# Kernel tuning notes

Measured on AMD Instinct MI355X. Metric: run time of the kernel, lower is better.

Reference implementation:

```python
import jax, jax.numpy as jnp
import numpy as np

TEMP = 0.05          # self.temp
NUM_LABELED = 15080  # SysuDataset bank size


def setup_inputs() -> dict:
    key = jax.random.key(0)
    k1, k2, k3, k4, k5 = jax.random.split(key, 5)
    B, D, L = 512, 2048, NUM_LABELED
    f = jax.random.normal(k1, (B, D), jnp.float32)
    features = f / jnp.linalg.norm(f, axis=1, keepdims=True)  # L2-normalized embeddings
    fk = jax.random.normal(k2, (B, D), jnp.float32)
    features_k = fk / jnp.linalg.norm(fk, axis=1, keepdims=True)
    gt_labels = jax.random.randint(k3, (B, 5), 0, L)   # last column = pid index
    gt_labels_k = jax.random.randint(k4, (B, 5), 0, L)
    bank = jax.random.normal(k5, (L, D), jnp.float32)
    bank_features = bank / jnp.linalg.norm(bank, axis=1, keepdims=True)
    return {"features": features, "features_k": features_k,
            "gt_labels": gt_labels, "gt_labels_k": gt_labels_k,
            "bank_features": bank_features}


def reference(features, features_k, gt_labels, gt_labels_k, bank_features):
    # pids = cat([i[:, -1] for i in gt_labels]); all >= 0 by construction, so the
    # pids > -1 filter is an identity (static shapes under jit).
    pids = gt_labels[:, -1]                                  # [B]
    # HM.forward: inputs.mm(features.t()), then /= temp
    sim_all = (features @ bank_features.T) / TEMP            # [B, L]
    # segment-mean of logits grouped by memory label (labels == arange -> identity,
    # kept for faithfulness to the index_add / nums normalization in the source)
    labels = jnp.arange(NUM_LABELED)
    sim = jax.ops.segment_sum(sim_all.T, labels, num_segments=NUM_LABELED)  # [L, B]
    nums = jax.ops.segment_sum(jnp.ones((NUM_LABELED, 1), jnp.float32),
                               labels, num_segments=NUM_LABELED)            # [L, 1]
    sim = sim / nums
    logits = sim.T                                           # [B, L]
    logp = jax.nn.log_softmax(logits, axis=-1)
    loss = -jnp.mean(jnp.take_along_axis(logp, pids[:, None], axis=1))
    return loss
```

## Files before the change

### kernel.cpp

```cpp
#include <hip/hip_runtime.h>
#include <hip/hip_bf16.h>

#define M_ROWS 512
#define N_COLS 15080
#define K_DIM  2048
#define BM 128
#define BN 128
#define BKF 64
#define NT 118
#define KSTEPS (K_DIM / BKF)
#define SCALE 20.0f

typedef _Float16 f16x8 __attribute__((ext_vector_type(8)));
typedef float    f32x4 __attribute__((ext_vector_type(4)));

extern "C" __global__ __launch_bounds__(512, 4)
void k_gemm_lse(const float* __restrict__ A,
                const float* __restrict__ Bk,
                const int*   __restrict__ gt,
                float* __restrict__ pm,
                float* __restrict__ ps,
                float* __restrict__ tv)
{
    __shared__ __align__(16) ushort lds[16384];

    const int t  = threadIdx.x;
    const int bx = blockIdx.x;

    int mi, nt;
    if (bx < 448) {
        const int slot = bx & 7;
        const int rest = bx >> 3;
        mi = rest & 3;
        nt = (rest >> 2) * 8 + slot;
    } else {
        const int r2 = bx - 448;
        mi = r2 & 3;
        nt = 112 + (r2 >> 2);
    }
    const int rowA0 = mi * BM;
    const int rowB0 = nt * BN;

    int arow[2], ag[2];
#pragma unroll
    for (int i = 0; i < 2; i++) { int G = t + i * 512; arow[i] = G >> 3; ag[i] = G & 7; }

    float4 ra[4], rb[4];
    auto LOAD = [&](int kt) {
#pragma unroll
        for (int i = 0; i < 2; i++) {
            const float* pa = A + (size_t)(rowA0 + arow[i]) * K_DIM + kt * BKF + ag[i] * 8;
            ra[2 * i]     = *(const float4*)(pa);
            ra[2 * i + 1] = *(const float4*)(pa + 4);
            const int br = rowB0 + arow[i];
            if (br < N_COLS) {
                const float* pb = Bk + (size_t)br * K_DIM + kt * BKF + ag[i] * 8;
                rb[2 * i]     = *(const float4*)(pb);
                rb[2 * i + 1] = *(const float4*)(pb + 4);
            } else {
                rb[2 * i]     = make_float4(0.f, 0.f, 0.f, 0.f);
                rb[2 * i + 1] = make_float4(0.f, 0.f, 0.f, 0.f);
            }
        }
    };
    auto STORE = [&]() {
#pragma unroll
        for (int i = 0; i < 2; i++) {
            const int ba = (arow[i] * 128 + ag[i] * 16) ^ ((arow[i] & 7) << 4);
            f16x8 ha, hb;
            float4 x = ra[2 * i], y = ra[2 * i + 1];
            ha[0] = (_Float16)x.x; ha[1] = (_Float16)x.y; ha[2] = (_Float16)x.z; ha[3] = (_Float16)x.w;
            ha[4] = (_Float16)y.x; ha[5] = (_Float16)y.y; ha[6] = (_Float16)y.z; ha[7] = (_Float16)y.w;
            x = rb[2 * i]; y = rb[2 * i + 1];
            hb[0] = (_Float16)x.x; hb[1] = (_Float16)x.y; hb[2] = (_Float16)x.z; hb[3] = (_Float16)x.w;
            hb[4] = (_Float16)y.x; hb[5] = (_Float16)y.y; hb[6] = (_Float16)y.z; hb[7] = (_Float16)y.w;
            *(f16x8*)((char*)lds + ba)         = ha;
            *(f16x8*)((char*)lds + 16384 + ba) = hb;
        }
    };

    const int lane = t & 63;
    const int wid  = t >> 6;
    const int wm = wid >> 2, wn = wid & 3;
    const int q = lane >> 4, r = lane & 15;
    int aaddr[4][2], baddr[2][2];
#pragma unroll
    for (int m = 0; m < 4; m++) {
        const int rowa = wm * 64 + m * 16 + r;
#pragma unroll
        for (int ks = 0; ks < 2; ks++)
            aaddr[m][ks] = (rowa * 128 + ks * 64 + q * 16) ^ ((rowa & 7) << 4);
    }
#pragma unroll
    for (int n = 0; n < 2; n++) {
        const int rowb = wn * 32 + n * 16 + r;
#pragma unroll
        for (int ks = 0; ks < 2; ks++)
            baddr[n][ks] = 16384 + ((rowb * 128 + ks * 64 + q * 16) ^ ((rowb & 7) << 4));
    }

    f32x4 acc[4][2];
    const f32x4 zero = {0.f, 0.f, 0.f, 0.f};
#pragma unroll
    for (int m = 0; m < 4; m++)
#pragma unroll
        for (int n = 0; n < 2; n++) acc[m][n] = zero;

    LOAD(0);
    for (int kt = 0; kt < KSTEPS; kt++) {
        __syncthreads();
        STORE();
        __syncthreads();
        if (kt + 1 < KSTEPS) LOAD(kt + 1);

        f16x8 bf[2][2];
#pragma unroll
        for (int n = 0; n < 2; n++)
#pragma unroll
            for (int ks = 0; ks < 2; ks++)
                bf[n][ks] = *(const f16x8*)((const char*)lds + baddr[n][ks]);
#pragma unroll
        for (int m = 0; m < 4; m++) {
            const f16x8 af0 = *(const f16x8*)((const char*)lds + aaddr[m][0]);
            const f16x8 af1 = *(const f16x8*)((const char*)lds + aaddr[m][1]);
#pragma unroll
            for (int n = 0; n < 2; n++) {
                acc[m][n] = __builtin_amdgcn_mfma_f32_16x16x32_f16(af0, bf[n][0], acc[m][n], 0, 0, 0);
                acc[m][n] = __builtin_amdgcn_mfma_f32_16x16x32_f16(af1, bf[n][1], acc[m][n], 0, 0, 0);
            }
        }
    }

    __syncthreads();
    float* redm = (float*)lds;
    float* reds = ((float*)lds) + 512;

#pragma unroll
    for (int m = 0; m < 4; m++) {
#pragma unroll
        for (int j = 0; j < 4; j++) {
            const int lrow = wm * 64 + m * 16 + q * 4 + j;
            const int grow = rowA0 + lrow;
            const int pid  = gt[grow * 5 + 4];
            float sv[2];
            float mx = -INFINITY;
#pragma unroll
            for (int n = 0; n < 2; n++) {
                const int gc = rowB0 + wn * 32 + n * 16 + r;
                float s = SCALE * acc[m][n][j];
                s = (gc < N_COLS) ? s : -INFINITY;
                sv[n] = s;
                mx = fmaxf(mx, s);
                if (gc == pid) tv[grow] = s;
            }
#pragma unroll
            for (int d = 1; d < 16; d <<= 1) mx = fmaxf(mx, __shfl_xor(mx, d, 16));
            float se = 0.f;
#pragma unroll
            for (int n = 0; n < 2; n++) se += __expf(sv[n] - mx);
#pragma unroll
            for (int d = 1; d < 16; d <<= 1) se += __shfl_xor(se, d, 16);
            if (r == 0) { redm[wn * 128 + lrow] = mx; reds[wn * 128 + lrow] = se; }
        }
    }
    __syncthreads();
    if (t < 128) {
        float Mv = -INFINITY;
#pragma unroll
        for (int c = 0; c < 4; c++) Mv = fmaxf(Mv, redm[c * 128 + t]);
        float Sv = 0.f;
#pragma unroll
        for (int c = 0; c < 4; c++) Sv += reds[c * 128 + t] * __expf(redm[c * 128 + t] - Mv);
        pm[(rowA0 + t) * NT + nt] = Mv;
        ps[(rowA0 + t) * NT + nt] = Sv;
    }
}

extern "C" __global__ __launch_bounds__(128)
void k_rowlse(const float* __restrict__ pm,
              const float* __restrict__ ps,
              const float* __restrict__ tv,
              float* __restrict__ rowloss)
{
    const int b = blockIdx.x;
    const int i = threadIdx.x;
    __shared__ float wred[4];

    const float m = (i < NT) ? pm[b * NT + i] : -INFINITY;
    const float s = (i < NT) ? ps[b * NT + i] : 0.f;

    float M = m;
#pragma unroll
    for (int d = 1; d < 64; d <<= 1) M = fmaxf(M, __shfl_xor(M, d, 64));
    if ((i & 63) == 0) wred[i >> 6] = M;
    __syncthreads();
    M = fmaxf(wred[0], wred[1]);
    __syncthreads();

    float e = (i < NT) ? s * __expf(m - M) : 0.f;
#pragma unroll
    for (int d = 1; d < 64; d <<= 1) e += __shfl_xor(e, d, 64);
    if ((i & 63) == 0) wred[i >> 6] = e;
    __syncthreads();
    if (i == 0) {
        const float S = wred[0] + wred[1];
        rowloss[b] = M + logf(S) - tv[b];
    }
}

extern "C" __global__ __launch_bounds__(512)
void k_final(const float* __restrict__ rowloss, float* __restrict__ out)
{
    __shared__ float red[512];
    const int b = threadIdx.x;
    red[b] = rowloss[b];
    __syncthreads();
    for (int s = 256; s > 0; s >>= 1) {
        if (b < s) red[b] += red[b + s];
        __syncthreads();
    }
    if (b == 0) out[0] = red[0] / 512.0f;
}

extern "C" void kernel_launch(void* const* d_in, const int* in_sizes, int n_in,
                              void* d_out, int out_size, void* d_ws, size_t ws_size,
                              hipStream_t stream)
{
    const float* feat = (const float*)d_in[0];
    const int*   gt   = (const int*)d_in[2];
    const float* bank = (const float*)d_in[4];

    float* pm = (float*)d_ws;
    float* ps = pm + 512 * NT;
    float* tv = ps + 512 * NT;
    float* rl = tv + 512;

    k_gemm_lse<<<dim3(4 * NT), 512, 0, stream>>>(feat, bank, gt, pm, ps, tv);
    k_rowlse<<<dim3(512), 128, 0, stream>>>(pm, ps, tv, rl);
    k_final<<<dim3(1), 512, 0, stream>>>(rl, (float*)d_out);
}
```

Measured before the change: 250.1 us.

## Split GEMM along K into two slices and move LSE into separate reduction pass

Adds a split-K GEMM kernel that computes two K halves as separate workgroups (944 blocks of 256 threads, 4x4 MFMA tiles per wave) and writes raw partial logits to a padded workspace. A new row kernel sums the two partials, applies the scale and does an online log-sum-exp plus target lookup. The aim is more workgroups and better CU fill than the 472-block fused kernel. The cost is writing and rereading about 62 MB of partials through global memory, and the path only runs if the workspace is large enough.

```diff
diff --git a/kernel.cpp b/kernel.cpp
--- a/kernel.cpp
+++ b/kernel.cpp
@@ -3,16 +3,196 @@
 
 #define M_ROWS 512
 #define N_COLS 15080
+#define N_PAD  15104
 #define K_DIM  2048
 #define BM 128
 #define BN 128
 #define BKF 64
 #define NT 118
-#define KSTEPS (K_DIM / BKF)
 #define SCALE 20.0f
+
+#define KS 2
+#define KSLICE (K_DIM / KS)
+#define KSTEPS_SK (KSLICE / BKF)
 
 typedef _Float16 f16x8 __attribute__((ext_vector_type(8)));
 typedef float    f32x4 __attribute__((ext_vector_type(4)));
+
+extern "C" __global__ __launch_bounds__(256, 2)
+void k_gemm_sk(const float* __restrict__ A,
+               const float* __restrict__ Bk,
+               float* __restrict__ part)
+{
+    __shared__ __align__(16) ushort lds[16384];
+
+    const int t  = threadIdx.x;
+    const int bx = blockIdx.x;
+
+    const int wgid  = (bx & 7) * 118 + (bx >> 3);
+    const int mi    = wgid & 3;
+    const int group = wgid >> 2;
+    const int nt    = group >> 1;
+    const int ks    = group & 1;
+    const int rowA0 = mi * BM;
+    const int rowB0 = nt * BN;
+    const int kbase = ks * KSLICE;
+    float* outp = part + (size_t)ks * M_ROWS * N_PAD;
+
+    int arow[4], ag[4];
+#pragma unroll
+    for (int i = 0; i < 4; i++) { int G = t + i * 256; arow[i] = G >> 3; ag[i] = G & 7; }
+
+    float4 ra[8], rb[8];
+    auto LOAD = [&](int kt) {
+#pragma unroll
+        for (int i = 0; i < 4; i++) {
+            const float* pa = A + (size_t)(rowA0 + arow[i]) * K_DIM + kbase + kt * BKF + ag[i] * 8;
+            ra[2 * i]     = *(const float4*)(pa);
+            ra[2 * i + 1] = *(const float4*)(pa + 4);
+            const int br = rowB0 + arow[i];
+            if (br < N_COLS) {
+                const float* pb = Bk + (size_t)br * K_DIM + kbase + kt * BKF + ag[i] * 8;
+                rb[2 * i]     = *(const float4*)(pb);
+                rb[2 * i + 1] = *(const float4*)(pb + 4);
+            } else {
+                rb[2 * i]     = make_float4(0.f, 0.f, 0.f, 0.f);
+                rb[2 * i + 1] = make_float4(0.f, 0.f, 0.f, 0.f);
+            }
+        }
+    };
+    auto STORE = [&]() {
+#pragma unroll
+        for (int i = 0; i < 4; i++) {
+            const int ba = (arow[i] * 128 + ag[i] * 16) ^ ((arow[i] & 7) << 4);
+            f16x8 ha, hb;
+            float4 x = ra[2 * i], y = ra[2 * i + 1];
+            ha[0] = (_Float16)x.x; ha[1] = (_Float16)x.y; ha[2] = (_Float16)x.z; ha[3] = (_Float16)x.w;
+            ha[4] = (_Float16)y.x; ha[5] = (_Float16)y.y; ha[6] = (_Float16)y.z; ha[7] = (_Float16)y.w;
+            x = rb[2 * i]; y = rb[2 * i + 1];
+            hb[0] = (_Float16)x.x; hb[1] = (_Float16)x.y; hb[2] = (_Float16)x.z; hb[3] = (_Float16)x.w;
+            hb[4] = (_Float16)y.x; hb[5] = (_Float16)y.y; hb[6] = (_Float16)y.z; hb[7] = (_Float16)y.w;
+            *(f16x8*)((char*)lds + ba)         = ha;
+            *(f16x8*)((char*)lds + 16384 + ba) = hb;
+        }
+    };
+
+    const int lane = t & 63;
+    const int wid  = t >> 6;
+    const int wm = wid >> 1, wn = wid & 1;
+    const int q = lane >> 4, r = lane & 15;
+    int aaddr[4][2], baddr[4][2];
+#pragma unroll
+    for (int m = 0; m < 4; m++) {
+        const int rowa = wm * 64 + m * 16 + r;
+        const int rowb = wn * 64 + m * 16 + r;
+#pragma unroll
+        for (int kss = 0; kss < 2; kss++) {
+            aaddr[m][kss] = (rowa * 128 + kss * 64 + q * 16) ^ ((rowa & 7) << 4);
+            baddr[m][kss] = 16384 + ((rowb * 128 + kss * 64 + q * 16) ^ ((rowb & 7) << 4));
+        }
+    }
+
+    f32x4 acc[4][4];
+    const f32x4 zero = {0.f, 0.f, 0.f, 0.f};
+#pragma unroll
+    for (int m = 0; m < 4; m++)
+#pragma unroll
+        for (int n = 0; n < 4; n++) acc[m][n] = zero;
+
+    LOAD(0);
+    for (int kt = 0; kt < KSTEPS_SK; kt++) {
+        __syncthreads();
+        STORE();
+        __syncthreads();
+        if (kt + 1 < KSTEPS_SK) LOAD(kt + 1);
+
+        f16x8 bf[4][2];
+#pragma unroll
+        for (int n = 0; n < 4; n++)
+#pragma unroll
+            for (int kss = 0; kss < 2; kss++)
+                bf[n][kss] = *(const f16x8*)((const char*)lds + baddr[n][kss]);
+#pragma unroll
+        for (int m = 0; m < 4; m++) {
+            const f16x8 af0 = *(const f16x8*)((const char*)lds + aaddr[m][0]);
+            const f16x8 af1 = *(const f16x8*)((const char*)lds + aaddr[m][1]);
+#pragma unroll
+            for (int n = 0; n < 4; n++) {
+                acc[m][n] = __builtin_amdgcn_mfma_f32_16x16x32_f16(af0, bf[n][0], acc[m][n], 0, 0, 0);
+                acc[m][n] = __builtin_amdgcn_mfma_f32_16x16x32_f16(af1, bf[n][1], acc[m][n], 0, 0, 0);
+            }
+        }
+    }
+
+#pragma unroll
+    for (int m = 0; m < 4; m++)
+#pragma unroll
+        for (int j = 0; j < 4; j++) {
+            const int grow = rowA0 + wm * 64 + m * 16 + q * 4 + j;
+            float* rowp = outp + (size_t)grow * N_PAD + rowB0 + wn * 64 + r;
+#pragma unroll
+            for (int n = 0; n < 4; n++) rowp[n * 16] = acc[m][n][j];
+        }
+}
+
+extern "C" __global__ __launch_bounds__(256)
+void k_lse(const float* __restrict__ part,
+           const int*   __restrict__ gt,
+           float* __restrict__ rowloss)
+{
+    const int b = blockIdx.x;
+    const int t = threadIdx.x;
+    __shared__ float lm[4], ls[4];
+
+    const float4* p0 = (const float4*)(part + (size_t)b * N_PAD);
+    const float4* p1 = (const float4*)(part + (size_t)(M_ROWS + b) * N_PAD);
+
+    float m = -1e30f, s = 0.f;
+    for (int c = t; c < 3770; c += 256) {
+        const float4 a = p0[c], d = p1[c];
+        const float x0 = SCALE * (a.x + d.x);
+        const float x1 = SCALE * (a.y + d.y);
+        const float x2 = SCALE * (a.z + d.z);
+        const float x3 = SCALE * (a.w + d.w);
+        const float mx = fmaxf(fmaxf(x0, x1), fmaxf(x2, x3));
+        if (mx > m) { s *= __expf(m - mx); m = mx; }
+        s += __expf(x0 - m) + __expf(x1 - m) + __expf(x2 - m) + __expf(x3 - m);
+    }
+#pragma unroll
+    for (int d = 1; d < 64; d <<= 1) {
+        const float om = __shfl_xor(m, d, 64);
+        const float os = __shfl_xor(s, d, 64);
+        const float nm = fmaxf(m, om);
+        s = s * __expf(m - nm) + os * __expf(om - nm);
+        m = nm;
+    }
+    if ((t & 63) == 0) { lm[t >> 6] = m; ls[t >> 6] = s; }
+    __syncthreads();
+    if (t == 0) {
+        float M = fmaxf(fmaxf(lm[0], lm[1]), fmaxf(lm[2], lm[3]));
+        float S = 0.f;
+#pragma unroll
+        for (int w = 0; w < 4; w++) S += ls[w] * __expf(lm[w] - M);
+        const int pid = gt[b * 5 + 4];
+        const float tgt = SCALE * (part[(size_t)b * N_PAD + pid] +
+                                   part[(size_t)(M_ROWS + b) * N_PAD + pid]);
+        rowloss[b] = M + logf(S) - tgt;
+    }
+}
+
+extern "C" __global__ __launch_bounds__(512)
+void k_final(const float* __restrict__ rowloss, float* __restrict__ out)
+{
+    __shared__ float red[512];
+    const int b = threadIdx.x;
+    red[b] = rowloss[b];
+    __syncthreads();
+    for (int s = 256; s > 0; s >>= 1) {
+        if (b < s) red[b] += red[b + s];
+        __syncthreads();
+    }
+    if (b == 0) out[0] = red[0] / 512.0f;
+}
 
 extern "C" __global__ __launch_bounds__(512, 4)
 void k_gemm_lse(const float* __restrict__ A,
@@ -26,7 +206,6 @@
 
     const int t  = threadIdx.x;
     const int bx = blockIdx.x;
-
     int mi, nt;
     if (bx < 448) {
         const int slot = bx & 7;
@@ -88,15 +267,15 @@
     for (int m = 0; m < 4; m++) {
         const int rowa = wm * 64 + m * 16 + r;
 #pragma unroll
-        for (int ks = 0; ks < 2; ks++)
-            aaddr[m][ks] = (rowa * 128 + ks * 64 + q * 16) ^ ((rowa & 7) << 4);
+        for (int kss = 0; kss < 2; kss++)
+            aaddr[m][kss] = (rowa * 128 + kss * 64 + q * 16) ^ ((rowa & 7) << 4);
     }
 #pragma unroll
     for (int n = 0; n < 2; n++) {
         const int rowb = wn * 32 + n * 16 + r;
 #pragma unroll
-        for (int ks = 0; ks < 2; ks++)
-            baddr[n][ks] = 16384 + ((rowb * 128 + ks * 64 + q * 16) ^ ((rowb & 7) << 4));
+        for (int kss = 0; kss < 2; kss++)
+            baddr[n][kss] = 16384 + ((rowb * 128 + kss * 64 + q * 16) ^ ((rowb & 7) << 4));
     }
 
     f32x4 acc[4][2];
@@ -107,18 +286,18 @@
         for (int n = 0; n < 2; n++) acc[m][n] = zero;
 
     LOAD(0);
-    for (int kt = 0; kt < KSTEPS; kt++) {
+    for (int kt = 0; kt < (K_DIM / BKF); kt++) {
         __syncthreads();
         STORE();
         __syncthreads();
-        if (kt + 1 < KSTEPS) LOAD(kt + 1);
+        if (kt + 1 < (K_DIM / BKF)) LOAD(kt + 1);
 
         f16x8 bf[2][2];
 #pragma unroll
         for (int n = 0; n < 2; n++)
 #pragma unroll
-            for (int ks = 0; ks < 2; ks++)
-                bf[n][ks] = *(const f16x8*)((const char*)lds + baddr[n][ks]);
+            for (int kss = 0; kss < 2; kss++)
+                bf[n][kss] = *(const f16x8*)((const char*)lds + baddr[n][kss]);
 #pragma unroll
         for (int m = 0; m < 4; m++) {
             const f16x8 af0 = *(const f16x8*)((const char*)lds + aaddr[m][0]);
@@ -208,20 +387,6 @@
     }
 }
 
-extern "C" __global__ __launch_bounds__(512)
-void k_final(const float* __restrict__ rowloss, float* __restrict__ out)
-{
-    __shared__ float red[512];
-    const int b = threadIdx.x;
-    red[b] = rowloss[b];
-    __syncthreads();
-    for (int s = 256; s > 0; s >>= 1) {
-        if (b < s) red[b] += red[b + s];
-        __syncthreads();
-    }
-    if (b == 0) out[0] = red[0] / 512.0f;
-}
-
 extern "C" void kernel_launch(void* const* d_in, const int* in_sizes, int n_in,
                               void* d_out, int out_size, void* d_ws, size_t ws_size,
                               hipStream_t stream)
@@ -230,12 +395,20 @@
     const int*   gt   = (const int*)d_in[2];
     const float* bank = (const float*)d_in[4];
 
-    float* pm = (float*)d_ws;
-    float* ps = pm + 512 * NT;
-    float* tv = ps + 512 * NT;
-    float* rl = tv + 512;
-
-    k_gemm_lse<<<dim3(4 * NT), 512, 0, stream>>>(feat, bank, gt, pm, ps, tv);
-    k_rowlse<<<dim3(512), 128, 0, stream>>>(pm, ps, tv, rl);
-    k_final<<<dim3(1), 512, 0, stream>>>(rl, (float*)d_out);
-}
+    const size_t need = (size_t)KS * M_ROWS * N_PAD * 4 + 512 * 4;
+    if (ws_size >= need) {
+        float* part = (float*)d_ws;
+        float* rl   = part + (size_t)KS * M_ROWS * N_PAD;
+        k_gemm_sk<<<dim3(8 * NT), 256, 0, stream>>>(feat, bank, part);
+        k_lse<<<dim3(M_ROWS), 256, 0, stream>>>(part, gt, rl);
+        k_final<<<dim3(1), 512, 0, stream>>>(rl, (float*)d_out);
+    } else {
+        float* pm = (float*)d_ws;
+        float* ps = pm + 512 * NT;
+        float* tv = ps + 512 * NT;
+        float* rl = tv + 512;
+        k_gemm_lse<<<dim3(4 * NT), 512, 0, stream>>>(feat, bank, gt, pm, ps, tv);
+        k_rowlse<<<dim3(512), 128, 0, stream>>>(pm, ps, tv, rl);
+        k_final<<<dim3(1), 512, 0, stream>>>(rl, (float*)d_out);
+    }
+}
```

Result: slower. 260.5 us (+4.1%).

## Pre-convert inputs to fp16 and use async global-to-LDS double-buffered GEMM

Applied to the files above, without the earlier changes.

Adds a conversion kernel that writes fp16 copies of the bank (zero-padded to a multiple of the tile) and the features into workspace. A new GEMM kernel then streams these fp16 tiles straight into LDS with global_load_lds into two buffers, so the load of the next k-step overlaps compute. It also uses 256 threads with a 64x64 warp tile. The aim is to halve the GEMM's global read traffic and remove the register round trip and per-tile conversion. The cost is an extra pass over the fp32 bank. The old path is kept as a fallback when the workspace is too small.

```diff
diff --git a/kernel.cpp b/kernel.cpp
--- a/kernel.cpp
+++ b/kernel.cpp
@@ -8,132 +8,142 @@
 #define BN 128
 #define BKF 64
 #define NT 118
-#define KSTEPS (K_DIM / BKF)
+#define KSTEPS 32
 #define SCALE 20.0f
+
+#define BANK_PAD_ROWS 15104
+#define BANK_PAD_E (30932992ull)
+#define FEAT_E     (1048576ull)
+#define NG_CVT     (3997696ull)
 
 typedef _Float16 f16x8 __attribute__((ext_vector_type(8)));
 typedef float    f32x4 __attribute__((ext_vector_type(4)));
 
-extern "C" __global__ __launch_bounds__(512, 4)
-void k_gemm_lse(const float* __restrict__ A,
-                const float* __restrict__ Bk,
-                const int*   __restrict__ gt,
-                float* __restrict__ pm,
-                float* __restrict__ ps,
-                float* __restrict__ tv)
-{
-    __shared__ __align__(16) ushort lds[16384];
+#define GLD_LDS16(gp, lp) __builtin_amdgcn_global_load_lds( \
+    (const __attribute__((address_space(1))) void*)(gp),    \
+    (__attribute__((address_space(3))) void*)(lp), 16, 0, 0)
+
+extern "C" __global__ __launch_bounds__(256)
+void k_cvt(const float* __restrict__ feat, const float* __restrict__ bank,
+           _Float16* __restrict__ out)
+{
+    const size_t stride = (size_t)gridDim.x * 256;
+    for (size_t g = (size_t)blockIdx.x * 256 + threadIdx.x; g < NG_CVT; g += stride) {
+        const size_t e = g * 8;
+        f16x8 h;
+        if (e < BANK_PAD_E) {
+            const int row = (int)(e >> 11);
+            if (row < N_COLS) {
+                const float4 x = *(const float4*)(bank + e);
+                const float4 y = *(const float4*)(bank + e + 4);
+                h[0] = (_Float16)x.x; h[1] = (_Float16)x.y; h[2] = (_Float16)x.z; h[3] = (_Float16)x.w;
+                h[4] = (_Float16)y.x; h[5] = (_Float16)y.y; h[6] = (_Float16)y.z; h[7] = (_Float16)y.w;
+            } else {
+                h = (f16x8)(_Float16)0.0f;
+            }
+        } else {
+            const size_t e2 = e - BANK_PAD_E;
+            const float4 x = *(const float4*)(feat + e2);
+            const float4 y = *(const float4*)(feat + e2 + 4);
+            h[0] = (_Float16)x.x; h[1] = (_Float16)x.y; h[2] = (_Float16)x.z; h[3] = (_Float16)x.w;
+            h[4] = (_Float16)y.x; h[5] = (_Float16)y.y; h[6] = (_Float16)y.z; h[7] = (_Float16)y.w;
+        }
+        *(f16x8*)(out + e) = h;
+    }
+}
+
+extern "C" __global__ __launch_bounds__(256, 2)
+void k_gemm16(const _Float16* __restrict__ A16,
+              const _Float16* __restrict__ B16,
+              const int*      __restrict__ gt,
+              float* __restrict__ pm,
+              float* __restrict__ ps,
+              float* __restrict__ tv)
+{
+    __shared__ __align__(16) char lds[65536];
 
     const int t  = threadIdx.x;
     const int bx = blockIdx.x;
 
     int mi, nt;
-    if (bx < 448) {
-        const int slot = bx & 7;
-        const int rest = bx >> 3;
-        mi = rest & 3;
-        nt = (rest >> 2) * 8 + slot;
-    } else {
-        const int r2 = bx - 448;
-        mi = r2 & 3;
-        nt = 112 + (r2 >> 2);
-    }
+    if (bx < 448) { const int slot = bx & 7; const int rest = bx >> 3;
+                    mi = rest & 3; nt = (rest >> 2) * 8 + slot; }
+    else          { const int r2 = bx - 448; mi = r2 & 3; nt = 112 + (r2 >> 2); }
     const int rowA0 = mi * BM;
     const int rowB0 = nt * BN;
 
-    int arow[2], ag[2];
-#pragma unroll
-    for (int i = 0; i < 2; i++) { int G = t + i * 512; arow[i] = G >> 3; ag[i] = G & 7; }
-
-    float4 ra[4], rb[4];
-    auto LOAD = [&](int kt) {
-#pragma unroll
-        for (int i = 0; i < 2; i++) {
-            const float* pa = A + (size_t)(rowA0 + arow[i]) * K_DIM + kt * BKF + ag[i] * 8;
-            ra[2 * i]     = *(const float4*)(pa);
-            ra[2 * i + 1] = *(const float4*)(pa + 4);
-            const int br = rowB0 + arow[i];
-            if (br < N_COLS) {
-                const float* pb = Bk + (size_t)br * K_DIM + kt * BKF + ag[i] * 8;
-                rb[2 * i]     = *(const float4*)(pb);
-                rb[2 * i + 1] = *(const float4*)(pb + 4);
-            } else {
-                rb[2 * i]     = make_float4(0.f, 0.f, 0.f, 0.f);
-                rb[2 * i + 1] = make_float4(0.f, 0.f, 0.f, 0.f);
-            }
+    const int lane = t & 63, w = t >> 6;
+    const int lr = lane >> 3, gg = lane & 7;
+    const size_t aE0 = (size_t)(rowA0 + w * 32 + lr) * K_DIM + (size_t)((gg ^ lr) * 8);
+    const size_t bE0 = (size_t)(rowB0 + w * 32 + lr) * K_DIM + (size_t)((gg ^ lr) * 8);
+    const char* aP0 = (const char*)(A16 + aE0);
+    const char* bP0 = (const char*)(B16 + bE0);
+    const int ldsW = w * 4096;
+
+    auto STAGE = [&](int kt, int sel) {
+        const int   dofs = sel * 32768;
+        const size_t ko  = (size_t)kt * 128;
+#pragma unroll
+        for (int j = 0; j < 4; j++) {
+            GLD_LDS16(aP0 + (size_t)j * 32768 + ko, lds + dofs + ldsW + j * 1024);
+            GLD_LDS16(bP0 + (size_t)j * 32768 + ko, lds + dofs + 16384 + ldsW + j * 1024);
         }
     };
-    auto STORE = [&]() {
-#pragma unroll
-        for (int i = 0; i < 2; i++) {
-            const int ba = (arow[i] * 128 + ag[i] * 16) ^ ((arow[i] & 7) << 4);
-            f16x8 ha, hb;
-            float4 x = ra[2 * i], y = ra[2 * i + 1];
-            ha[0] = (_Float16)x.x; ha[1] = (_Float16)x.y; ha[2] = (_Float16)x.z; ha[3] = (_Float16)x.w;
-            ha[4] = (_Float16)y.x; ha[5] = (_Float16)y.y; ha[6] = (_Float16)y.z; ha[7] = (_Float16)y.w;
-            x = rb[2 * i]; y = rb[2 * i + 1];
-            hb[0] = (_Float16)x.x; hb[1] = (_Float16)x.y; hb[2] = (_Float16)x.z; hb[3] = (_Float16)x.w;
-            hb[4] = (_Float16)y.x; hb[5] = (_Float16)y.y; hb[6] = (_Float16)y.z; hb[7] = (_Float16)y.w;
-            *(f16x8*)((char*)lds + ba)         = ha;
-            *(f16x8*)((char*)lds + 16384 + ba) = hb;
-        }
-    };
-
-    const int lane = t & 63;
-    const int wid  = t >> 6;
-    const int wm = wid >> 2, wn = wid & 3;
+
+    const int wm = w >> 1, wn = w & 1;
     const int q = lane >> 4, r = lane & 15;
-    int aaddr[4][2], baddr[2][2];
+    int aaddr[4][2], baddr[4][2];
 #pragma unroll
     for (int m = 0; m < 4; m++) {
         const int rowa = wm * 64 + m * 16 + r;
-#pragma unroll
-        for (int ks = 0; ks < 2; ks++)
+        const int rowb = wn * 64 + m * 16 + r;
+#pragma unroll
+        for (int ks = 0; ks < 2; ks++) {
             aaddr[m][ks] = (rowa * 128 + ks * 64 + q * 16) ^ ((rowa & 7) << 4);
-    }
-#pragma unroll
-    for (int n = 0; n < 2; n++) {
-        const int rowb = wn * 32 + n * 16 + r;
-#pragma unroll
-        for (int ks = 0; ks < 2; ks++)
-            baddr[n][ks] = 16384 + ((rowb * 128 + ks * 64 + q * 16) ^ ((rowb & 7) << 4));
-    }
-
-    f32x4 acc[4][2];
+            baddr[m][ks] = 16384 + ((rowb * 128 + ks * 64 + q * 16) ^ ((rowb & 7) << 4));
+        }
+    }
+
+    f32x4 acc[4][4];
     const f32x4 zero = {0.f, 0.f, 0.f, 0.f};
 #pragma unroll
     for (int m = 0; m < 4; m++)
 #pragma unroll
-        for (int n = 0; n < 2; n++) acc[m][n] = zero;
-
-    LOAD(0);
-    for (int kt = 0; kt < KSTEPS; kt++) {
-        __syncthreads();
-        STORE();
-        __syncthreads();
-        if (kt + 1 < KSTEPS) LOAD(kt + 1);
-
-        f16x8 bf[2][2];
-#pragma unroll
-        for (int n = 0; n < 2; n++)
+        for (int n = 0; n < 4; n++) acc[m][n] = zero;
+
+    auto COMPUTE = [&](int sel) {
+        const char* bb = lds + sel * 32768;
+        f16x8 bf[4][2];
+#pragma unroll
+        for (int n = 0; n < 4; n++)
 #pragma unroll
             for (int ks = 0; ks < 2; ks++)
-                bf[n][ks] = *(const f16x8*)((const char*)lds + baddr[n][ks]);
+                bf[n][ks] = *(const f16x8*)(bb + baddr[n][ks]);
 #pragma unroll
         for (int m = 0; m < 4; m++) {
-            const f16x8 af0 = *(const f16x8*)((const char*)lds + aaddr[m][0]);
-            const f16x8 af1 = *(const f16x8*)((const char*)lds + aaddr[m][1]);
-#pragma unroll
-            for (int n = 0; n < 2; n++) {
+            const f16x8 af0 = *(const f16x8*)(bb + aaddr[m][0]);
+            const f16x8 af1 = *(const f16x8*)(bb + aaddr[m][1]);
+#pragma unroll
+            for (int n = 0; n < 4; n++) {
                 acc[m][n] = __builtin_amdgcn_mfma_f32_16x16x32_f16(af0, bf[n][0], acc[m][n], 0, 0, 0);
                 acc[m][n] = __builtin_amdgcn_mfma_f32_16x16x32_f16(af1, bf[n][1], acc[m][n], 0, 0, 0);
             }
         }
-    }
+    };
+
+    STAGE(0, 0);
+    __syncthreads();
+#pragma unroll 2
+    for (int kt = 0; kt < KSTEPS - 1; kt++) {
+        STAGE(kt + 1, (kt + 1) & 1);
+        COMPUTE(kt & 1);
+        __syncthreads();
+    }
+    COMPUTE((KSTEPS - 1) & 1);
 
     __syncthreads();
     float* redm = (float*)lds;
-    float* reds = ((float*)lds) + 512;
+    float* reds = ((float*)lds) + 256;
 
 #pragma unroll
     for (int m = 0; m < 4; m++) {
@@ -142,11 +152,11 @@
             const int lrow = wm * 64 + m * 16 + q * 4 + j;
             const int grow = rowA0 + lrow;
             const int pid  = gt[grow * 5 + 4];
-            float sv[2];
+            float sv[4];
             float mx = -INFINITY;
 #pragma unroll
-            for (int n = 0; n < 2; n++) {
-                const int gc = rowB0 + wn * 32 + n * 16 + r;
+            for (int n = 0; n < 4; n++) {
+                const int gc = rowB0 + wn * 64 + n * 16 + r;
                 float s = SCALE * acc[m][n][j];
                 s = (gc < N_COLS) ? s : -INFINITY;
                 sv[n] = s;
@@ -157,7 +167,7 @@
             for (int d = 1; d < 16; d <<= 1) mx = fmaxf(mx, __shfl_xor(mx, d, 16));
             float se = 0.f;
 #pragma unroll
-            for (int n = 0; n < 2; n++) se += __expf(sv[n] - mx);
+            for (int n = 0; n < 4; n++) se += __expf(sv[n] - mx);
 #pragma unroll
             for (int d = 1; d < 16; d <<= 1) se += __shfl_xor(se, d, 16);
             if (r == 0) { redm[wn * 128 + lrow] = mx; reds[wn * 128 + lrow] = se; }
@@ -165,12 +175,10 @@
     }
     __syncthreads();
     if (t < 128) {
-        float Mv = -INFINITY;
-#pragma unroll
-        for (int c = 0; c < 4; c++) Mv = fmaxf(Mv, redm[c * 128 + t]);
-        float Sv = 0.f;
-#pragma unroll
-        for (int c = 0; c < 4; c++) Sv += reds[c * 128 + t] * __expf(redm[c * 128 + t] - Mv);
+        const float m0 = redm[t], m1 = redm[128 + t];
+        const float s0 = reds[t], s1 = reds[128 + t];
+        const float Mv = fmaxf(m0, m1);
+        const float Sv = s0 * __expf(m0 - Mv) + s1 * __expf(m1 - Mv);
         pm[(rowA0 + t) * NT + nt] = Mv;
         ps[(rowA0 + t) * NT + nt] = Sv;
     }
@@ -222,6 +230,135 @@
     if (b == 0) out[0] = red[0] / 512.0f;
 }
 
+extern "C" __global__ __launch_bounds__(512, 4)
+void k_gemm_lse(const float* __restrict__ A,
+                const float* __restrict__ Bk,
+                const int*   __restrict__ gt,
+                float* __restrict__ pm, float* __restrict__ ps,
+                float* __restrict__ tv)
+{
+    __shared__ __align__(16) ushort lds[16384];
+    const int t  = threadIdx.x;
+    const int bx = blockIdx.x;
+    int mi, nt;
+    if (bx < 448) { const int slot = bx & 7; const int rest = bx >> 3;
+                    mi = rest & 3; nt = (rest >> 2) * 8 + slot; }
+    else          { const int r2 = bx - 448; mi = r2 & 3; nt = 112 + (r2 >> 2); }
+    const int rowA0 = mi * BM, rowB0 = nt * BN;
+
+    int arow[2], ag[2];
+#pragma unroll
+    for (int i = 0; i < 2; i++) { int G = t + i * 512; arow[i] = G >> 3; ag[i] = G & 7; }
+    float4 ra[4], rb[4];
+    auto LOAD = [&](int kt) {
+#pragma unroll
+        for (int i = 0; i < 2; i++) {
+            const float* pa = A + (size_t)(rowA0 + arow[i]) * K_DIM + kt * BKF + ag[i] * 8;
+            ra[2*i] = *(const float4*)(pa); ra[2*i+1] = *(const float4*)(pa + 4);
+            const int br = rowB0 + arow[i];
+            if (br < N_COLS) {
+                const float* pb = Bk + (size_t)br * K_DIM + kt * BKF + ag[i] * 8;
+                rb[2*i] = *(const float4*)(pb); rb[2*i+1] = *(const float4*)(pb + 4);
+            } else { rb[2*i] = make_float4(0,0,0,0); rb[2*i+1] = make_float4(0,0,0,0); }
+        }
+    };
+    auto STORE = [&]() {
+#pragma unroll
+        for (int i = 0; i < 2; i++) {
+            const int ba = (arow[i] * 128 + ag[i] * 16) ^ ((arow[i] & 7) << 4);
+            f16x8 ha, hb;
+            float4 x = ra[2*i], y = ra[2*i+1];
+            ha[0]=(_Float16)x.x; ha[1]=(_Float16)x.y; ha[2]=(_Float16)x.z; ha[3]=(_Float16)x.w;
+            ha[4]=(_Float16)y.x; ha[5]=(_Float16)y.y; ha[6]=(_Float16)y.z; ha[7]=(_Float16)y.w;
+            x = rb[2*i]; y = rb[2*i+1];
+            hb[0]=(_Float16)x.x; hb[1]=(_Float16)x.y; hb[2]=(_Float16)x.z; hb[3]=(_Float16)x.w;
+            hb[4]=(_Float16)y.x; hb[5]=(_Float16)y.y; hb[6]=(_Float16)y.z; hb[7]=(_Float16)y.w;
+            *(f16x8*)((char*)lds + ba) = ha;
+            *(f16x8*)((char*)lds + 16384 + ba) = hb;
+        }
+    };
+    const int lane = t & 63, wid = t >> 6;
+    const int wm = wid >> 2, wn = wid & 3;
+    const int q = lane >> 4, r = lane & 15;
+    int aaddr[4][2], baddr[2][2];
+#pragma unroll
+    for (int m = 0; m < 4; m++) { const int rowa = wm*64 + m*16 + r;
+#pragma unroll
+        for (int ks = 0; ks < 2; ks++) aaddr[m][ks] = (rowa*128 + ks*64 + q*16) ^ ((rowa&7)<<4); }
+#pragma unroll
+    for (int n = 0; n < 2; n++) { const int rowb = wn*32 + n*16 + r;
+#pragma unroll
+        for (int ks = 0; ks < 2; ks++) baddr[n][ks] = 16384 + ((rowb*128 + ks*64 + q*16) ^ ((rowb&7)<<4)); }
+
+    f32x4 acc[4][2];
+    const f32x4 zero = {0.f,0.f,0.f,0.f};
+#pragma unroll
+    for (int m = 0; m < 4; m++)
+#pragma unroll
+        for (int n = 0; n < 2; n++) acc[m][n] = zero;
+
+    LOAD(0);
+    for (int kt = 0; kt < KSTEPS; kt++) {
+        __syncthreads(); STORE(); __syncthreads();
+        if (kt + 1 < KSTEPS) LOAD(kt + 1);
+        f16x8 bf[2][2];
+#pragma unroll
+        for (int n = 0; n < 2; n++)
+#pragma unroll
+            for (int ks = 0; ks < 2; ks++) bf[n][ks] = *(const f16x8*)((const char*)lds + baddr[n][ks]);
+#pragma unroll
+        for (int m = 0; m < 4; m++) {
+            const f16x8 af0 = *(const f16x8*)((const char*)lds + aaddr[m][0]);
+            const f16x8 af1 = *(const f16x8*)((const char*)lds + aaddr[m][1]);
+#pragma unroll
+            for (int n = 0; n < 2; n++) {
+                acc[m][n] = __builtin_amdgcn_mfma_f32_16x16x32_f16(af0, bf[n][0], acc[m][n], 0,0,0);
+                acc[m][n] = __builtin_amdgcn_mfma_f32_16x16x32_f16(af1, bf[n][1], acc[m][n], 0,0,0);
+            }
+        }
+    }
+    __syncthreads();
+    float* redm = (float*)lds;
+    float* reds = ((float*)lds) + 512;
+#pragma unroll
+    for (int m = 0; m < 4; m++) {
+#pragma unroll
+        for (int j = 0; j < 4; j++) {
+            const int lrow = wm*64 + m*16 + q*4 + j;
+            const int grow = rowA0 + lrow;
+            const int pid  = gt[grow*5 + 4];
+            float sv[2]; float mx = -INFINITY;
+#pragma unroll
+            for (int n = 0; n < 2; n++) {
+                const int gc = rowB0 + wn*32 + n*16 + r;
+                float s = SCALE * acc[m][n][j];
+                s = (gc < N_COLS) ? s : -INFINITY;
+                sv[n] = s; mx = fmaxf(mx, s);
+                if (gc == pid) tv[grow] = s;
+            }
+#pragma unroll
+            for (int d = 1; d < 16; d <<= 1) mx = fmaxf(mx, __shfl_xor(mx, d, 16));
+            float se = 0.f;
+#pragma unroll
+            for (int n = 0; n < 2; n++) se += __expf(sv[n] - mx);
+#pragma unroll
+            for (int d = 1; d < 16; d <<= 1) se += __shfl_xor(se, d, 16);
+            if (r == 0) { redm[wn*128 + lrow] = mx; reds[wn*128 + lrow] = se; }
+        }
+    }
+    __syncthreads();
+    if (t < 128) {
+        float Mv = -INFINITY;
+#pragma unroll
+        for (int c = 0; c < 4; c++) Mv = fmaxf(Mv, redm[c*128 + t]);
+        float Sv = 0.f;
+#pragma unroll
+        for (int c = 0; c < 4; c++) Sv += reds[c*128 + t] * __expf(redm[c*128 + t] - Mv);
+        pm[(rowA0 + t) * NT + nt] = Mv;
+        ps[(rowA0 + t) * NT + nt] = Sv;
+    }
+}
+
 extern "C" void kernel_launch(void* const* d_in, const int* in_sizes, int n_in,
                               void* d_out, int out_size, void* d_ws, size_t ws_size,
                               hipStream_t stream)
@@ -230,12 +367,25 @@
     const int*   gt   = (const int*)d_in[2];
     const float* bank = (const float*)d_in[4];
 
-    float* pm = (float*)d_ws;
-    float* ps = pm + 512 * NT;
-    float* tv = ps + 512 * NT;
-    float* rl = tv + 512;
-
-    k_gemm_lse<<<dim3(4 * NT), 512, 0, stream>>>(feat, bank, gt, pm, ps, tv);
-    k_rowlse<<<dim3(512), 128, 0, stream>>>(pm, ps, tv, rl);
-    k_final<<<dim3(1), 512, 0, stream>>>(rl, (float*)d_out);
-}
+    const size_t NEED = (BANK_PAD_E + FEAT_E) * 2 + (size_t)512 * NT * 4 * 2 + 512 * 4 * 2;
+    if (ws_size >= NEED) {
+        _Float16* bank16 = (_Float16*)d_ws;
+        _Float16* feat16 = bank16 + BANK_PAD_E;
+        float* pm = (float*)(feat16 + FEAT_E);
+        float* ps = pm + 512 * NT;
+        float* tv = ps + 512 * NT;
+        float* rl = tv + 512;
+        k_cvt<<<dim3(2048), 256, 0, stream>>>(feat, bank, bank16);
+        k_gemm16<<<dim3(4 * NT), 256, 0, stream>>>(feat16, bank16, gt, pm, ps, tv);
+        k_rowlse<<<dim3(512), 128, 0, stream>>>(pm, ps, tv, rl);
+        k_final<<<dim3(1), 512, 0, stream>>>(rl, (float*)d_out);
+    } else {
+        float* pm = (float*)d_ws;
+        float* ps = pm + 512 * NT;
+        float* tv = ps + 512 * NT;
+        float* rl = tv + 512;
+        k_gemm_lse<<<dim3(4 * NT), 512, 0, stream>>>(feat, bank, gt, pm, ps, tv);
+        k_rowlse<<<dim3(512), 128, 0, stream>>>(pm, ps, tv, rl);
+        k_final<<<dim3(1), 512, 0, stream>>>(rl, (float*)d_out);
+    }
+}
```

Result: faster. 239.5 us (-4.3%).
